# Kernel tuning notes

Hardware: AMD Instinct MI355X
Metric: run time of the kernel (lower is better)

## Reference

```python
import jax, jax.numpy as jnp
import numpy as np

INCH, OUTCH, H, W = 1536, 256, 60, 60
B = 4


def resize_bilinear_align_corners(x, oh, ow):
    """F.interpolate(x, (oh, ow), mode='bilinear', align_corners=True) for NCHW x."""
    Bx, C, Hx, Wx = x.shape
    ys = jnp.linspace(0.0, Hx - 1.0, oh)
    xs = jnp.linspace(0.0, Wx - 1.0, ow)
    y0 = jnp.floor(ys).astype(jnp.int32)
    x0 = jnp.floor(xs).astype(jnp.int32)
    y1 = jnp.minimum(y0 + 1, Hx - 1)
    x1 = jnp.minimum(x0 + 1, Wx - 1)
    wy = (ys - y0.astype(x.dtype))[:, None]   # [oh,1]
    wx = (xs - x0.astype(x.dtype))[None, :]   # [1,ow]
    g = lambda yi, xi: x[:, :, yi][:, :, :, xi]  # [B,C,oh,ow]
    top = (1.0 - wx) * g(y0, x0) + wx * g(y0, x1)
    bot = (1.0 - wx) * g(y1, x0) + wx * g(y1, x1)
    return (1.0 - wy) * top + wy * bot


def setup_inputs() -> dict:
    key = jax.random.key(0)
    ks = jax.random.split(key, 8)
    feat_supp = jax.random.normal(ks[0], (B, INCH, H, W), dtype=jnp.float32)
    feat_query = jax.random.normal(ks[1], (B, INCH, H, W), dtype=jnp.float32)
    mask_supp = jax.random.uniform(ks[2], (B, 1, 473, 473), dtype=jnp.float32)
    scale = 0.02
    W_lpf = jax.random.normal(ks[3], (OUTCH, INCH), dtype=jnp.float32) * scale   # shared_LPF 1x1 conv
    W_supp = jax.random.normal(ks[4], (OUTCH, INCH), dtype=jnp.float32) * scale  # supp_linear
    W_query = jax.random.normal(ks[5], (OUTCH, INCH), dtype=jnp.float32) * scale # query_linear
    W_final = jax.random.normal(ks[6], (OUTCH, 2 * OUTCH), dtype=jnp.float32) * scale
    b_final = jax.random.normal(ks[7], (OUTCH,), dtype=jnp.float32) * scale
    return {"feat_supp": feat_supp, "feat_query": feat_query, "mask_supp": mask_supp,
            "W_lpf": W_lpf, "W_supp": W_supp, "W_query": W_query,
            "W_final": W_final, "b_final": b_final}


def conv1x1(x, Wm):
    # x: [b,c,h,w], Wm: [o,c]
    return jnp.einsum('bchw,oc->bohw', x, Wm)


def reference(feat_supp, feat_query, mask_supp, W_lpf, W_supp, W_query, W_final, b_final):
    b, d, h, w = feat_supp.shape
    hw = h * w
    v_supp = conv1x1(feat_supp, W_lpf)    # [b,256,h,w]
    v_query = conv1x1(feat_query, W_lpf)  # [b,256,h,w]
    k = conv1x1(feat_supp, W_supp).transpose(0, 2, 3, 1).reshape(b, hw, -1)   # [b,hw,256]
    q = conv1x1(feat_query, W_query).transpose(0, 2, 3, 1).reshape(b, hw, -1) # [b,hw,256]
    attn = jnp.einsum('bqd,bkd->bqk', q, k)  # [b,hw,hw]
    fg_mask = resize_bilinear_align_corners(mask_supp, h, w)  # [b,1,h,w]
    bg_suppress = ((1.0 - fg_mask) * -999.0).reshape(b, 1, hw)
    attn = jax.nn.softmax(attn + bg_suppress, axis=-1)
    vs = v_supp.transpose(0, 2, 3, 1).reshape(b, hw, -1)      # [b,hw,256]
    out = jnp.einsum('bqk,bkd->bqd', attn, vs)                # [b,hw,256]
    out = out.reshape(b, h, w, -1).transpose(0, 3, 1, 2)      # [b,256,h,w]
    cat = jnp.concatenate([out, v_query], axis=1)             # [b,512,h,w]
    final = jax.nn.relu(conv1x1(cat, W_final) + b_final[None, :, None, None])
    return final, attn.reshape(b, h, w, h, w)
```

## Files before the change

### kernel.cpp

```cpp
#include <hip/hip_runtime.h>
#include <stdint.h>

typedef unsigned short u16;
typedef _Float16 h16;
typedef __attribute__((ext_vector_type(4))) float f32x4;
typedef __attribute__((ext_vector_type(8))) short s16x8;
typedef __attribute__((ext_vector_type(8))) _Float16 h16x8;
typedef __attribute__((ext_vector_type(4))) _Float16 h16x4;
typedef __attribute__((ext_vector_type(4))) unsigned short u16x4;
typedef __attribute__((ext_vector_type(8))) unsigned short u16x8;

#define HW   3600
#define HWP  3648
#define DIM  256
#define CIN  1536
#define LDK  72
#define NCB  58
#define PSH  15.0f

__device__ __forceinline__ u16 f2bf(float f) {
  uint32_t u = __float_as_uint(f);
  uint32_t r = (u + 0x7fffu + ((u >> 16) & 1u)) >> 16;
  return (u16)r;
}
__device__ __forceinline__ float bf2f(u16 h) { return __uint_as_float((uint32_t)h << 16); }

template<int MR, int NR>
__device__ __forceinline__ void mfma_tile(const h16 (*As)[LDK], const h16 (*Bs)[LDK],
                                          int lane, int wr, int wc, f32x4 acc[MR][NR]) {
#pragma unroll
  for (int ks = 0; ks < 2; ++ks) {
    const int ko = ks * 32 + ((lane >> 4) << 3);
    h16x8 af[MR], bv[NR];
#pragma unroll
    for (int m = 0; m < MR; ++m) af[m] = *(const h16x8*)&As[wr + m * 16 + (lane & 15)][ko];
#pragma unroll
    for (int n = 0; n < NR; ++n) bv[n] = *(const h16x8*)&Bs[wc + n * 16 + (lane & 15)][ko];
#pragma unroll
    for (int m = 0; m < MR; ++m)
#pragma unroll
      for (int n = 0; n < NR; ++n)
        acc[m][n] = __builtin_amdgcn_mfma_f32_16x16x32_f16(af[m], bv[n], acc[m][n], 0, 0, 0);
  }
}

template<int MR, int NR>
__device__ __forceinline__ void mfma_tile_bf(const u16 (*As)[LDK], const u16 (*Bs)[LDK],
                                             int lane, int wr, int wc, f32x4 acc[MR][NR]) {
#pragma unroll
  for (int ks = 0; ks < 2; ++ks) {
    const int ko = ks * 32 + ((lane >> 4) << 3);
    s16x8 af[MR], bv[NR];
#pragma unroll
    for (int m = 0; m < MR; ++m) af[m] = *(const s16x8*)&As[wr + m * 16 + (lane & 15)][ko];
#pragma unroll
    for (int n = 0; n < NR; ++n) bv[n] = *(const s16x8*)&Bs[wc + n * 16 + (lane & 15)][ko];
#pragma unroll
    for (int m = 0; m < MR; ++m)
#pragma unroll
      for (int n = 0; n < NR; ++n)
        acc[m][n] = __builtin_amdgcn_mfma_f32_16x16x32_bf16(af[m], bv[n], acc[m][n], 0, 0, 0);
  }
}

#define NW    (256 * 1536)
#define NWF   (256 * 512)
#define NPAD  (4 * 256 * 48)
#define NPREP (14400 + 3 * NW + NWF + NPAD)

__global__ __launch_bounds__(256) void k_prep(
    const float* __restrict__ mask, const float* __restrict__ Wlpf,
    const float* __restrict__ Wsupp, const float* __restrict__ Wquery,
    const float* __restrict__ Wfin,
    float* __restrict__ sup, h16* __restrict__ Wl16, h16* __restrict__ Ws16,
    h16* __restrict__ Wq16, h16* __restrict__ Wf16, u16* __restrict__ vs) {
  int i = blockIdx.x * 256 + threadIdx.x;
  if (i < 14400) {
    int b = i / HW, p = i % HW, py = p / 60, px = p % 60;
    float fg = mask[(size_t)b * 473 * 473 + (size_t)(py * 8) * 473 + px * 8];
    sup[i] = (1.0f - fg) * -999.0f;
  } else if (i < 14400 + NW) {
    int j = i - 14400; Wl16[j] = (h16)Wlpf[j];
  } else if (i < 14400 + 2 * NW) {
    int j = i - 14400 - NW; Ws16[j] = (h16)Wsupp[j];
  } else if (i < 14400 + 3 * NW) {
    int j = i - 14400 - 2 * NW; Wq16[j] = (h16)Wquery[j];
  } else if (i < 14400 + 3 * NW + NWF) {
    int j = i - 14400 - 3 * NW; Wf16[j] = (h16)Wfin[j];
  } else if (i < NPREP) {
    int j = i - 14400 - 3 * NW - NWF;
    int b = j / (256 * 48), rem = j % (256 * 48), d = rem / 48, kk = rem % 48;
    vs[((size_t)b * DIM + d) * HWP + 3600 + kk] = 0;
  }
}

__global__ __launch_bounds__(512, 4) void k_conv(
    const h16* __restrict__ Wl16, const h16* __restrict__ Ws16, const h16* __restrict__ Wq16,
    const float* __restrict__ featS, const float* __restrict__ featQ,
    u16* __restrict__ vs, h16* __restrict__ vq,
    h16* __restrict__ kbuf, h16* __restrict__ qbuf) {
  const int lin = blockIdx.x;
  const int xcd = lin & 7, slot = lin >> 3;
  const int ct = slot >> 1, rb = slot & 1;
  const int b = xcd & 3, isQ = xcd >> 2;
  const int colBase = ct * 128;
  const int tid = threadIdx.x, lane = tid & 63, wid = tid >> 6;
  const int wr = (wid >> 1) << 6, wc = (wid & 1) << 6;
  const h16* Wsel = (rb == 0) ? Wl16 : (isQ ? Wq16 : Ws16);
  const float* feat = (isQ ? featQ : featS) + (size_t)b * CIN * HW;

  __shared__ h16 As[256][LDK];
  __shared__ h16 Bs[128][LDK];
  f32x4 acc[4][4] = {};

  const int a_r = tid >> 3, a_kv = (tid & 7) << 3;
  const int b_n = tid & 127, b_kh = (tid >> 7) << 4;
  const int gnc = colBase + b_n;
  const int gn = gnc < HW ? gnc : HW - 1;

  s16x8 aR[4];
  float bR[16];
#pragma unroll
  for (int i = 0; i < 4; ++i)
    aR[i] = *(const s16x8*)&Wsel[(size_t)(a_r + i * 64) * CIN + a_kv];
#pragma unroll
  for (int j = 0; j < 16; ++j) bR[j] = feat[(size_t)(b_kh + j) * HW + gn];

  for (int kt = 0; kt < 24; ++kt) {
#pragma unroll
    for (int i = 0; i < 4; ++i) *(s16x8*)&As[a_r + i * 64][a_kv] = aR[i];
    {
      h16x8 h0, h1;
#pragma unroll
      for (int c = 0; c < 8; ++c) { h0[c] = (h16)bR[c]; h1[c] = (h16)bR[8 + c]; }
      *(h16x8*)&Bs[b_n][b_kh] = h0;
      *(h16x8*)&Bs[b_n][b_kh + 8] = h1;
    }
    if (kt < 23) {
      const int k0n = (kt + 1) * 64;
#pragma unroll
      for (int i = 0; i < 4; ++i)
        aR[i] = *(const s16x8*)&Wsel[(size_t)(a_r + i * 64) * CIN + k0n + a_kv];
#pragma unroll
      for (int j = 0; j < 16; ++j) bR[j] = feat[(size_t)(k0n + b_kh + j) * HW + gn];
    }
    __syncthreads();
    mfma_tile<4, 4>(As, Bs, lane, wr, wc, acc);
    __syncthreads();
  }

  if (rb == 0 && !isQ) {
    u16* dst = vs + (size_t)b * DIM * HWP;
#pragma unroll
    for (int m = 0; m < 4; ++m) {
      const int d0 = wr + m * 16 + ((lane >> 4) << 2);
#pragma unroll
      for (int n = 0; n < 4; ++n) {
        const int pix = colBase + wc + n * 16 + (lane & 15);
        if (pix < HW) {
#pragma unroll
          for (int r = 0; r < 4; ++r) dst[(size_t)(d0 + r) * HWP + pix] = f2bf(acc[m][n][r]);
        }
      }
    }
  } else {
    h16* dst = ((rb == 0) ? vq : (isQ ? qbuf : kbuf)) + (size_t)b * HW * DIM;
#pragma unroll
    for (int m = 0; m < 4; ++m) {
      const int d0 = wr + m * 16 + ((lane >> 4) << 2);
#pragma unroll
      for (int n = 0; n < 4; ++n) {
        const int pix = colBase + wc + n * 16 + (lane & 15);
        if (pix < HW) {
          h16x4 h = {(h16)acc[m][n][0], (h16)acc[m][n][1],
                     (h16)acc[m][n][2], (h16)acc[m][n][3]};
          *(h16x4*)&dst[(size_t)pix * DIM + d0] = h;
        }
      }
    }
  }
}

__global__ __launch_bounds__(256) void k_qk(
    const h16* __restrict__ qbuf, const h16* __restrict__ kbuf,
    const float* __restrict__ sup, u16* __restrict__ p, float* __restrict__ stat) {
  const int hwid = blockIdx.x;
  const int xcd = hwid & 7, pos = hwid >> 3;
  const int logical = (xcd < 4) ? xcd * 421 + pos : 1684 + (xcd - 4) * 420 + pos;
  const int b = logical / 841, rem = logical % 841;
  const int rt = rem / 29, ct = rem % 29;
  const int rowBase = rt * 128, colBase = ct * 128;
  const int tid = threadIdx.x, lane = tid & 63, wid = tid >> 6;
  const int wr = (wid >> 1) << 6, wc = (wid & 1) << 6;
  const h16* Aq = qbuf + (size_t)b * HW * DIM;
  const h16* Bk = kbuf + (size_t)b * HW * DIM;

  __shared__ __align__(16) char smem[128 * LDK * 2 * 2];
  h16 (*As)[LDK] = (h16(*)[LDK])smem;
  h16 (*Bs)[LDK] = (h16(*)[LDK])(smem + 128 * LDK * 2);
  u16 (*pC)[136] = (u16(*)[136])smem;

  f32x4 acc[4][4] = {};
  const int r0 = tid >> 3, kv8 = (tid & 7) << 3;

  int gaR[4], gbR[4];
#pragma unroll
  for (int i = 0; i < 4; ++i) {
    const int r = r0 + i * 32;
    int ga = rowBase + r; gaR[i] = ga < HW ? ga : HW - 1;
    int gb = colBase + r; gbR[i] = gb < HW ? gb : HW - 1;
  }
  s16x8 aR[4], bR[4];
#pragma unroll
  for (int i = 0; i < 4; ++i) {
    aR[i] = *(const s16x8*)(Aq + (size_t)gaR[i] * DIM + kv8);
    bR[i] = *(const s16x8*)(Bk + (size_t)gbR[i] * DIM + kv8);
  }

  for (int kt = 0; kt < 4; ++kt) {
#pragma unroll
    for (int i = 0; i < 4; ++i) {
      *(s16x8*)&As[r0 + i * 32][kv8] = aR[i];
      *(s16x8*)&Bs[r0 + i * 32][kv8] = bR[i];
    }
    if (kt < 3) {
      const int k0n = (kt + 1) * 64;
#pragma unroll
      for (int i = 0; i < 4; ++i) {
        aR[i] = *(const s16x8*)(Aq + (size_t)gaR[i] * DIM + k0n + kv8);
        bR[i] = *(const s16x8*)(Bk + (size_t)gbR[i] * DIM + k0n + kv8);
      }
    }
    __syncthreads();
    mfma_tile<4, 4>(As, Bs, lane, wr, wc, acc);
    __syncthreads();
  }

  float sup4[4]; int kp4[4];
#pragma unroll
  for (int n = 0; n < 4; ++n) {
    const int kp = colBase + wc + n * 16 + (lane & 15);
    kp4[n] = kp;
    sup4[n] = (kp < HW) ? sup[b * HW + kp] : 0.f;
  }
  float* st = stat + (size_t)(b * NCB + ct * 2 + (wc >> 6)) * HW;
#pragma unroll
  for (int m = 0; m < 4; ++m) {
#pragma unroll
    for (int r = 0; r < 4; ++r) {
      float pr[4];
      float ls = 0.f;
#pragma unroll
      for (int n = 0; n < 4; ++n) {
        pr[n] = (kp4[n] < HW) ? __expf(acc[m][n][r] + sup4[n] - PSH) : 0.f;
        ls += pr[n];
      }
#pragma unroll
      for (int off = 1; off < 16; off <<= 1) ls += __shfl_xor(ls, off);
      const int rl = wr + m * 16 + ((lane >> 4) << 2) + r;
      if ((lane & 15) == 0) {
        const int qp = rowBase + rl;
        if (qp < HW) st[qp] = ls;
      }
#pragma unroll
      for (int n = 0; n < 4; ++n) pC[rl][wc + n * 16 + (lane & 15)] = f2bf(pr[n]);
    }
  }
  __syncthreads();
  u16* pB = p + (size_t)b * HW * HWP;
#pragma unroll
  for (int pass = 0; pass < 8; ++pass) {
    const int rl = pass * 16 + (tid >> 4);
    const int qp = rowBase + rl;
    const int col = colBase + (tid & 15) * 8;
    if (qp < HW && col < HW) {
      u16x8 v = *(const u16x8*)&pC[rl][(tid & 15) * 8];
      *(u16x8*)&pB[(size_t)qp * HWP + col] = v;
    }
  }
}

__global__ __launch_bounds__(256) void k_rowsum(const float* __restrict__ stat,
                                                float* __restrict__ invS) {
  const int i = blockIdx.x * 256 + threadIdx.x;
  if (i >= 4 * HW) return;
  const int b = i / HW, row = i % HW;
  const float* s = stat + (size_t)b * NCB * HW + row;
  float S = 0.f;
  for (int c = 0; c < NCB; ++c) S += s[(size_t)c * HW];
  invS[i] = 1.0f / S;
}

__global__ __launch_bounds__(256) void k_pvsm(
    const u16* __restrict__ p, const u16* __restrict__ vs,
    const float* __restrict__ invS, float* __restrict__ attn, float* __restrict__ part) {
  const int lin = blockIdx.x;
  const int xcd = lin & 7, slot = lin >> 3;
  const int b = xcd >> 1, sphalf = xcd & 1;
  const int split = sphalf * 2 + (slot & 1);
  const int rt = slot >> 1;
  const int rowBase = rt * 64;
  const int tid = threadIdx.x, lane = tid & 63, wid = tid >> 6;
  const int wc = wid << 6;
  const u16* pB = p + (size_t)b * HW * HWP;
  const u16* Bv = vs + (size_t)b * DIM * HWP;
  float* Ab = attn + (size_t)b * HW * HW;

  __shared__ u16 As[64][LDK];
  __shared__ u16 Bs[256][LDK];
  __shared__ float Ir[64];
  f32x4 acc[4][4] = {};

  if (tid < 64) {
    const int ga = rowBase + tid;
    Ir[tid] = (ga < HW) ? invS[b * HW + ga] : 0.f;
  }
  __syncthreads();

  const int a_r = tid >> 4, a_kv = (tid & 15) << 2;
  const int b_r = tid >> 3, b_kv = (tid & 7) << 3;
  const int t0 = split * 15, t1 = (split == 3) ? 57 : split * 15 + 15;

  u16x4 pR[4];
  s16x8 vR[8];
  {
    const int kc = t0 * 64 + a_kv;
#pragma unroll
    for (int i = 0; i < 4; ++i) {
      const int ga = rowBase + a_r + i * 16;
      pR[i] = (u16x4){0, 0, 0, 0};
      if (ga < HW && kc < HW) pR[i] = *(const u16x4*)&pB[(size_t)ga * HWP + kc];
    }
#pragma unroll
    for (int i = 0; i < 8; ++i)
      vR[i] = *(const s16x8*)&Bv[(size_t)(b_r + i * 32) * HWP + t0 * 64 + b_kv];
  }

  for (int kt = t0; kt < t1; ++kt) {
    const int kc = kt * 64 + a_kv;
#pragma unroll
    for (int i = 0; i < 4; ++i) {
      const int r = a_r + i * 16;
      const int ga = rowBase + r;
      if (ga < HW && kc < HW) {
        const float I = Ir[r];
        f32x4 w;
#pragma unroll
        for (int c = 0; c < 4; ++c) w[c] = bf2f(pR[i][c]) * I;
        __builtin_nontemporal_store(w, (f32x4*)(Ab + (size_t)ga * HW + kc));
      }
      *(u16x4*)&As[r][a_kv] = pR[i];
    }
#pragma unroll
    for (int i = 0; i < 8; ++i) *(s16x8*)&Bs[b_r + i * 32][b_kv] = vR[i];
    if (kt + 1 < t1) {
      const int kcn = (kt + 1) * 64 + a_kv;
#pragma unroll
      for (int i = 0; i < 4; ++i) {
        const int ga = rowBase + a_r + i * 16;
        pR[i] = (u16x4){0, 0, 0, 0};
        if (ga < HW && kcn < HW) pR[i] = *(const u16x4*)&pB[(size_t)ga * HWP + kcn];
      }
#pragma unroll
      for (int i = 0; i < 8; ++i)
        vR[i] = *(const s16x8*)&Bv[(size_t)(b_r + i * 32) * HWP + (kt + 1) * 64 + b_kv];
    }
    __syncthreads();
    mfma_tile_bf<4, 4>(As, Bs, lane, 0, wc, acc);
    __syncthreads();
  }
  float* dst = part + (size_t)(split * 4 + b) * HW * DIM;
#pragma unroll
  for (int m = 0; m < 4; ++m) {
    const int pix0 = rowBase + m * 16 + ((lane >> 4) << 2);
#pragma unroll
    for (int n = 0; n < 4; ++n) {
      const int d = wc + n * 16 + (lane & 15);
#pragma unroll
      for (int r = 0; r < 4; ++r)
        if (pix0 + r < HW) dst[(size_t)(pix0 + r) * DIM + d] = acc[m][n][r];
    }
  }
}

__global__ __launch_bounds__(256) void k_pvred(const float* __restrict__ part,
                                               const float* __restrict__ invS,
                                               h16* __restrict__ ov) {
  const size_t idx = (size_t)blockIdx.x * 256 + threadIdx.x;
  const size_t base = idx * 4;
  const size_t stride = (size_t)4 * HW * DIM;
  f32x4 s = *(const f32x4*)&part[base];
#pragma unroll
  for (int sp = 1; sp < 4; ++sp) s += *(const f32x4*)&part[sp * stride + base];
  const float I = invS[base / DIM];
  h16x4 h = {(h16)(s[0] * I), (h16)(s[1] * I), (h16)(s[2] * I), (h16)(s[3] * I)};
  *(h16x4*)&ov[base] = h;
}

__global__ __launch_bounds__(256) void k_final(
    const h16* __restrict__ ov, const h16* __restrict__ vq,
    const h16* __restrict__ Wf16, const float* __restrict__ bfin,
    float* __restrict__ outF) {
  const int tid = threadIdx.x, lane = tid & 63, wid = tid >> 6;
  const int wr = (wid >> 1) << 5, wc = (wid & 1) << 6;
  const int rowBase = blockIdx.x * 64;
  const int colBase = blockIdx.y * 128;
  const int b = blockIdx.z;
  const h16* Aov = ov + (size_t)b * HW * DIM;
  const h16* Avq = vq + (size_t)b * HW * DIM;

  __shared__ h16 As[64][LDK];
  __shared__ h16 Bs[128][LDK];
  f32x4 acc[2][4] = {};

  const int a_r = tid >> 3, a_kv = (tid & 7) << 3;
  int gaR[2];
#pragma unroll
  for (int i = 0; i < 2; ++i) {
    int ga = rowBase + a_r + i * 32; gaR[i] = ga < HW ? ga : HW - 1;
  }

  s16x8 aR[2], bR[4];
#pragma unroll
  for (int i = 0; i < 2; ++i)
    aR[i] = *(const s16x8*)(Aov + (size_t)gaR[i] * DIM + a_kv);
#pragma unroll
  for (int i = 0; i < 4; ++i)
    bR[i] = *(const s16x8*)(Wf16 + (size_t)(colBase + a_r + i * 32) * 512 + a_kv);

  for (int kt = 0; kt < 8; ++kt) {
#pragma unroll
    for (int i = 0; i < 2; ++i) *(s16x8*)&As[a_r + i * 32][a_kv] = aR[i];
#pragma unroll
    for (int i = 0; i < 4; ++i) *(s16x8*)&Bs[a_r + i * 32][a_kv] = bR[i];
    if (kt < 7) {
      const int k0n = (kt + 1) * 64;
      const h16* Asrc = (k0n < 256) ? Aov : Avq;
      const int ak = k0n & 255;
#pragma unroll
      for (int i = 0; i < 2; ++i)
        aR[i] = *(const s16x8*)(Asrc + (size_t)gaR[i] * DIM + ak + a_kv);
#pragma unroll
      for (int i = 0; i < 4; ++i)
        bR[i] = *(const s16x8*)(Wf16 + (size_t)(colBase + a_r + i * 32) * 512 + k0n + a_kv);
    }
    __syncthreads();
    mfma_tile<2, 4>(As, Bs, lane, wr, wc, acc);
    __syncthreads();
  }
  float* dst = outF + (size_t)b * DIM * HW;
#pragma unroll
  for (int n = 0; n < 4; ++n) {
    const int o = colBase + wc + n * 16 + (lane & 15);
    const float bb = bfin[o];
#pragma unroll
    for (int m = 0; m < 2; ++m) {
      const int pix0 = rowBase + wr + m * 16 + ((lane >> 4) << 2);
      if (pix0 < HW) {
        f32x4 v;
#pragma unroll
        for (int r = 0; r < 4; ++r) v[r] = fmaxf(acc[m][n][r] + bb, 0.f);
        *(f32x4*)(dst + (size_t)o * HW + pix0) = v;
      }
    }
  }
}

extern "C" void kernel_launch(void* const* d_in, const int* in_sizes, int n_in,
                              void* d_out, int out_size, void* d_ws, size_t ws_size,
                              hipStream_t stream) {
  (void)in_sizes; (void)n_in; (void)out_size; (void)ws_size;
  const float* featS  = (const float*)d_in[0];
  const float* featQ  = (const float*)d_in[1];
  const float* mask   = (const float*)d_in[2];
  const float* Wlpf   = (const float*)d_in[3];
  const float* Wsupp  = (const float*)d_in[4];
  const float* Wquery = (const float*)d_in[5];
  const float* Wfin   = (const float*)d_in[6];
  const float* bfin   = (const float*)d_in[7];

  float* outF = (float*)d_out;
  float* attn = outF + (size_t)4 * DIM * HW;

  char* w = (char*)d_ws;
  h16* qbuf = (h16*)w;  w += (size_t)4 * HW * DIM * 2;
  h16* kbuf = (h16*)w;  w += (size_t)4 * HW * DIM * 2;
  u16* vs   = (u16*)w;  w += (size_t)4 * DIM * HWP * 2;
  h16* vq   = (h16*)w;  w += (size_t)4 * HW * DIM * 2;
  h16* ov   = (h16*)w;  w += (size_t)4 * HW * DIM * 2;
  float* part = (float*)w;  w += (size_t)4 * 4 * HW * DIM * 4;
  u16* pbuf = (u16*)w;  w += (size_t)4 * HW * HWP * 2;
  h16* Wl16 = (h16*)w;  w += (size_t)NW * 2;
  h16* Ws16 = (h16*)w;  w += (size_t)NW * 2;
  h16* Wq16 = (h16*)w;  w += (size_t)NW * 2;
  h16* Wf16 = (h16*)w;  w += (size_t)NWF * 2;
  float* stat = (float*)w;  w += (size_t)4 * NCB * HW * 4;
  float* invS = (float*)w;  w += (size_t)4 * HW * 4;
  float* sup  = (float*)w;

  k_prep<<<dim3((NPREP + 255) / 256), 256, 0, stream>>>(
      mask, Wlpf, Wsupp, Wquery, Wfin, sup, Wl16, Ws16, Wq16, Wf16, vs);
  k_conv<<<dim3(464), 512, 0, stream>>>(Wl16, Ws16, Wq16, featS, featQ,
                                        vs, vq, kbuf, qbuf);
  k_qk<<<dim3(3364), 256, 0, stream>>>(qbuf, kbuf, sup, pbuf, stat);
  k_rowsum<<<dim3(57), 256, 0, stream>>>(stat, invS);
  k_pvsm<<<dim3(912), 256, 0, stream>>>(pbuf, vs, invS, attn, part);
  k_pvred<<<dim3(3600), 256, 0, stream>>>(part, invS, ov);
  k_final<<<dim3(57, 2, 4), 256, 0, stream>>>(ov, vq, Wf16, bfin, outF);
}
```

Baseline: 270.5 us.

## Read conv weights directly from global and fuse split-K reduction into final conv

The 1x1 conv kernel no longer stages the weight tile in shared memory. Each wave loads its f16 weight fragments straight from global memory into MFMA operands, and the feature tile is double-buffered in registers across two K-steps. Separately, the standalone k_pvred reduction kernel is removed: k_final now sums the four split-K partials, scales them by the inverse softmax row sum, and converts to f16 while loading its A operand. This saves a kernel launch and the round trip through the ov buffer, at the cost of more global weight traffic per wave and redundant partial reads across the column blocks of k_final.

```diff
diff --git a/kernel.cpp b/kernel.cpp
--- a/kernel.cpp
+++ b/kernel.cpp
@@ -60,6 +60,28 @@
 #pragma unroll
       for (int n = 0; n < NR; ++n)
         acc[m][n] = __builtin_amdgcn_mfma_f32_16x16x32_bf16(af[m], bv[n], acc[m][n], 0, 0, 0);
+  }
+}
+
+__device__ __forceinline__ void mfma_conv(const h16* __restrict__ Wfrag, int kbase,
+                                          const h16 (*Bs)[LDK], int lane, int wc,
+                                          f32x4 acc[4][4]) {
+#pragma unroll
+  for (int ks = 0; ks < 2; ++ks) {
+    const int kog = kbase + ks * 32;
+    const int kol = ks * 32 + ((lane >> 4) << 3);
+    h16x8 af[4], bv[4];
+#pragma unroll
+    for (int m = 0; m < 4; ++m)
+      af[m] = *(const h16x8*)(Wfrag + (size_t)(m * 16) * CIN + kog);
+#pragma unroll
+    for (int n = 0; n < 4; ++n)
+      bv[n] = *(const h16x8*)&Bs[wc + n * 16 + (lane & 15)][kol];
+#pragma unroll
+    for (int m = 0; m < 4; ++m)
+#pragma unroll
+      for (int n = 0; n < 4; ++n)
+        acc[m][n] = __builtin_amdgcn_mfma_f32_16x16x32_f16(af[m], bv[n], acc[m][n], 0, 0, 0);
   }
 }
 
@@ -108,44 +130,51 @@
   const int wr = (wid >> 1) << 6, wc = (wid & 1) << 6;
   const h16* Wsel = (rb == 0) ? Wl16 : (isQ ? Wq16 : Ws16);
   const float* feat = (isQ ? featQ : featS) + (size_t)b * CIN * HW;
-
-  __shared__ h16 As[256][LDK];
+  const h16* Wfrag = Wsel + (size_t)(wr + (lane & 15)) * CIN + ((lane >> 4) << 3);
+
   __shared__ h16 Bs[128][LDK];
   f32x4 acc[4][4] = {};
 
-  const int a_r = tid >> 3, a_kv = (tid & 7) << 3;
   const int b_n = tid & 127, b_kh = (tid >> 7) << 4;
   const int gnc = colBase + b_n;
   const int gn = gnc < HW ? gnc : HW - 1;
 
-  s16x8 aR[4];
-  float bR[16];
-#pragma unroll
-  for (int i = 0; i < 4; ++i)
-    aR[i] = *(const s16x8*)&Wsel[(size_t)(a_r + i * 64) * CIN + a_kv];
-#pragma unroll
-  for (int j = 0; j < 16; ++j) bR[j] = feat[(size_t)(b_kh + j) * HW + gn];
-
-  for (int kt = 0; kt < 24; ++kt) {
-#pragma unroll
-    for (int i = 0; i < 4; ++i) *(s16x8*)&As[a_r + i * 64][a_kv] = aR[i];
+  float b0[16], b1[16];
+#pragma unroll
+  for (int j = 0; j < 16; ++j) b0[j] = feat[(size_t)(b_kh + j) * HW + gn];
+#pragma unroll
+  for (int j = 0; j < 16; ++j) b1[j] = feat[(size_t)(64 + b_kh + j) * HW + gn];
+
+  for (int kt = 0; kt < 24; kt += 2) {
     {
       h16x8 h0, h1;
 #pragma unroll
-      for (int c = 0; c < 8; ++c) { h0[c] = (h16)bR[c]; h1[c] = (h16)bR[8 + c]; }
+      for (int c = 0; c < 8; ++c) { h0[c] = (h16)b0[c]; h1[c] = (h16)b0[8 + c]; }
       *(h16x8*)&Bs[b_n][b_kh] = h0;
       *(h16x8*)&Bs[b_n][b_kh + 8] = h1;
     }
-    if (kt < 23) {
-      const int k0n = (kt + 1) * 64;
-#pragma unroll
-      for (int i = 0; i < 4; ++i)
-        aR[i] = *(const s16x8*)&Wsel[(size_t)(a_r + i * 64) * CIN + k0n + a_kv];
-#pragma unroll
-      for (int j = 0; j < 16; ++j) bR[j] = feat[(size_t)(k0n + b_kh + j) * HW + gn];
-    }
-    __syncthreads();
-    mfma_tile<4, 4>(As, Bs, lane, wr, wc, acc);
+    if (kt + 2 < 24) {
+      const int k0n = (kt + 2) * 64;
+#pragma unroll
+      for (int j = 0; j < 16; ++j) b0[j] = feat[(size_t)(k0n + b_kh + j) * HW + gn];
+    }
+    __syncthreads();
+    mfma_conv(Wfrag, kt * 64, Bs, lane, wc, acc);
+    __syncthreads();
+    {
+      h16x8 h0, h1;
+#pragma unroll
+      for (int c = 0; c < 8; ++c) { h0[c] = (h16)b1[c]; h1[c] = (h16)b1[8 + c]; }
+      *(h16x8*)&Bs[b_n][b_kh] = h0;
+      *(h16x8*)&Bs[b_n][b_kh + 8] = h1;
+    }
+    if (kt + 3 < 24) {
+      const int k0n = (kt + 3) * 64;
+#pragma unroll
+      for (int j = 0; j < 16; ++j) b1[j] = feat[(size_t)(k0n + b_kh + j) * HW + gn];
+    }
+    __syncthreads();
+    mfma_conv(Wfrag, (kt + 1) * 64, Bs, lane, wc, acc);
     __syncthreads();
   }
 
@@ -383,47 +412,45 @@
   }
 }
 
-__global__ __launch_bounds__(256) void k_pvred(const float* __restrict__ part,
-                                               const float* __restrict__ invS,
-                                               h16* __restrict__ ov) {
-  const size_t idx = (size_t)blockIdx.x * 256 + threadIdx.x;
-  const size_t base = idx * 4;
-  const size_t stride = (size_t)4 * HW * DIM;
-  f32x4 s = *(const f32x4*)&part[base];
-#pragma unroll
-  for (int sp = 1; sp < 4; ++sp) s += *(const f32x4*)&part[sp * stride + base];
-  const float I = invS[base / DIM];
-  h16x4 h = {(h16)(s[0] * I), (h16)(s[1] * I), (h16)(s[2] * I), (h16)(s[3] * I)};
-  *(h16x4*)&ov[base] = h;
-}
-
 __global__ __launch_bounds__(256) void k_final(
-    const h16* __restrict__ ov, const h16* __restrict__ vq,
+    const float* __restrict__ part, const h16* __restrict__ vq,
     const h16* __restrict__ Wf16, const float* __restrict__ bfin,
-    float* __restrict__ outF) {
+    const float* __restrict__ invS, float* __restrict__ outF) {
   const int tid = threadIdx.x, lane = tid & 63, wid = tid >> 6;
   const int wr = (wid >> 1) << 5, wc = (wid & 1) << 6;
   const int rowBase = blockIdx.x * 64;
   const int colBase = blockIdx.y * 128;
   const int b = blockIdx.z;
-  const h16* Aov = ov + (size_t)b * HW * DIM;
   const h16* Avq = vq + (size_t)b * HW * DIM;
+  const size_t pstride = (size_t)4 * HW * DIM;
 
   __shared__ h16 As[64][LDK];
   __shared__ h16 Bs[128][LDK];
   f32x4 acc[2][4] = {};
 
   const int a_r = tid >> 3, a_kv = (tid & 7) << 3;
-  int gaR[2];
+  int gaR[2]; float IrT[2];
 #pragma unroll
   for (int i = 0; i < 2; ++i) {
     int ga = rowBase + a_r + i * 32; gaR[i] = ga < HW ? ga : HW - 1;
+    IrT[i] = invS[b * HW + gaR[i]];
   }
 
   s16x8 aR[2], bR[4];
 #pragma unroll
-  for (int i = 0; i < 2; ++i)
-    aR[i] = *(const s16x8*)(Aov + (size_t)gaR[i] * DIM + a_kv);
+  for (int i = 0; i < 2; ++i) {
+    const float* pb = part + ((size_t)b * HW + gaR[i]) * DIM + a_kv;
+    f32x4 s0 = *(const f32x4*)pb, s1 = *(const f32x4*)(pb + 4);
+#pragma unroll
+    for (int sp = 1; sp < 4; ++sp) {
+      s0 += *(const f32x4*)(pb + sp * pstride);
+      s1 += *(const f32x4*)(pb + sp * pstride + 4);
+    }
+    h16x8 h;
+#pragma unroll
+    for (int c = 0; c < 4; ++c) { h[c] = (h16)(s0[c] * IrT[i]); h[4 + c] = (h16)(s1[c] * IrT[i]); }
+    aR[i] = *(s16x8*)&h;
+  }
 #pragma unroll
   for (int i = 0; i < 4; ++i)
     bR[i] = *(const s16x8*)(Wf16 + (size_t)(colBase + a_r + i * 32) * 512 + a_kv);
@@ -435,11 +462,27 @@
     for (int i = 0; i < 4; ++i) *(s16x8*)&Bs[a_r + i * 32][a_kv] = bR[i];
     if (kt < 7) {
       const int k0n = (kt + 1) * 64;
-      const h16* Asrc = (k0n < 256) ? Aov : Avq;
-      const int ak = k0n & 255;
-#pragma unroll
-      for (int i = 0; i < 2; ++i)
-        aR[i] = *(const s16x8*)(Asrc + (size_t)gaR[i] * DIM + ak + a_kv);
+      if (k0n < 256) {
+#pragma unroll
+        for (int i = 0; i < 2; ++i) {
+          const float* pb = part + ((size_t)b * HW + gaR[i]) * DIM + k0n + a_kv;
+          f32x4 s0 = *(const f32x4*)pb, s1 = *(const f32x4*)(pb + 4);
+#pragma unroll
+          for (int sp = 1; sp < 4; ++sp) {
+            s0 += *(const f32x4*)(pb + sp * pstride);
+            s1 += *(const f32x4*)(pb + sp * pstride + 4);
+          }
+          h16x8 h;
+#pragma unroll
+          for (int c = 0; c < 4; ++c) { h[c] = (h16)(s0[c] * IrT[i]); h[4 + c] = (h16)(s1[c] * IrT[i]); }
+          aR[i] = *(s16x8*)&h;
+        }
+      } else {
+        const int ak = k0n - 256;
+#pragma unroll
+        for (int i = 0; i < 2; ++i)
+          aR[i] = *(const s16x8*)(Avq + (size_t)gaR[i] * DIM + ak + a_kv);
+      }
 #pragma unroll
       for (int i = 0; i < 4; ++i)
         bR[i] = *(const s16x8*)(Wf16 + (size_t)(colBase + a_r + i * 32) * 512 + k0n + a_kv);
@@ -487,7 +530,6 @@
   h16* kbuf = (h16*)w;  w += (size_t)4 * HW * DIM * 2;
   u16* vs   = (u16*)w;  w += (size_t)4 * DIM * HWP * 2;
   h16* vq   = (h16*)w;  w += (size_t)4 * HW * DIM * 2;
-  h16* ov   = (h16*)w;  w += (size_t)4 * HW * DIM * 2;
   float* part = (float*)w;  w += (size_t)4 * 4 * HW * DIM * 4;
   u16* pbuf = (u16*)w;  w += (size_t)4 * HW * HWP * 2;
   h16* Wl16 = (h16*)w;  w += (size_t)NW * 2;
@@ -505,6 +547,5 @@
   k_qk<<<dim3(3364), 256, 0, stream>>>(qbuf, kbuf, sup, pbuf, stat);
   k_rowsum<<<dim3(57), 256, 0, stream>>>(stat, invS);
   k_pvsm<<<dim3(912), 256, 0, stream>>>(pbuf, vs, invS, attn, part);
-  k_pvred<<<dim3(3600), 256, 0, stream>>>(part, invS, ov);
-  k_final<<<dim3(57, 2, 4), 256, 0, stream>>>(ov, vq, Wf16, bfin, outF);
-}
+  k_final<<<dim3(57, 2, 4), 256, 0, stream>>>(part, vq, Wf16, bfin, invS, outF);
+}
```

Result: slower. 517.4 us (+91.3%).
